# Kernel tuning notes

Hardware: AMD Instinct MI355X
Metric: run time of the kernel (lower is better)

The kernel has to match this reference:

```python
import jax, jax.numpy as jnp
import numpy as np

B, H_HIST, S_DIM, HID, G, K, A = 1024, 16384, 32, 64, 10, 4, 8


def setup_inputs() -> dict:
    key = jax.random.key(0)
    ks = jax.random.split(key, 12)
    inp = {
        'state_batch': jax.random.normal(ks[0], (B, S_DIM), jnp.float32),
        'state_history_batch': jax.random.normal(ks[1], (H_HIST, S_DIM), jnp.float32),
        'joint_action_history_batch': jax.random.normal(ks[2], (H_HIST, G, A), jnp.float32),
        # per-abstract-agent encoder MLP: Linear(S->H) + ReLU, Linear(H->H) + ReLU, Linear(H->H) + ReLU
        'W0': jax.random.normal(ks[3], (K, S_DIM, HID), jnp.float32) / np.sqrt(S_DIM),
        'b0': jax.random.normal(ks[4], (K, HID), jnp.float32) * 0.01,
        'W1': jax.random.normal(ks[5], (K, HID, HID), jnp.float32) / np.sqrt(HID),
        'b1': jax.random.normal(ks[6], (K, HID), jnp.float32) * 0.01,
        'W2': jax.random.normal(ks[7], (K, HID, HID), jnp.float32) / np.sqrt(HID),
        'b2': jax.random.normal(ks[8], (K, HID), jnp.float32) * 0.01,
        'assignment_matrix': jnp.ones((G, K), jnp.float32),
    }
    return inp


def _encode(x, W0, b0, W1, b1, W2, b2):
    # x: [N, S_DIM] shared across K encoders -> [K, N, HID]
    h = jax.nn.relu(jnp.einsum('ni,kio->kno', x, W0) + b0[:, None, :])
    h = jax.nn.relu(jnp.einsum('kni,kio->kno', h, W1) + b1[:, None, :])
    h = jax.nn.relu(jnp.einsum('kni,kio->kno', h, W2) + b2[:, None, :])
    return h


def reference(state_batch, state_history_batch, joint_action_history_batch,
              W0, b0, W1, b1, W2, b2, assignment_matrix):
    enc_s = _encode(state_batch, W0, b0, W1, b1, W2, b2)            # [K, B, HID]
    enc_h = _encode(state_history_batch, W0, b0, W1, b1, W2, b2)    # [K, H, HID]
    # per (abstract agent k, batch item b): softmax over history of <enc_h, enc_s>
    attn = jax.nn.softmax(jnp.einsum('khd,kbd->kbh', enc_h, enc_s), axis=-1)  # [K, B, H]
    # weighted action aggregation: [H,G,A] contracted over H
    abs_pred = jnp.einsum('kbh,hga->kbga', attn, joint_action_history_batch)  # [K, B, G, A]
    soft_assign = jax.nn.softmax(assignment_matrix, axis=-1)                  # [G, K]
    out = jnp.einsum('gk,kbga->bga', soft_assign, abs_pred)                   # [B, G, A]
    return out
```

## Files before the change

### kernel.cpp

```cpp
#include <hip/hip_runtime.h>
#include <stdint.h>

#define B_SZ 1024
#define H_SZ 16384
#define SD   32
#define HID  64
#define G_SZ 10
#define K_SZ 4
#define A_SZ 8
#define VA   80

typedef float f32x4  __attribute__((ext_vector_type(4)));
typedef short bf16x8 __attribute__((ext_vector_type(8)));

__device__ inline short f2bf(float a) {
    unsigned u = __float_as_uint(a);
    return (short)((u + 0x7FFFu + ((u >> 16) & 1u)) >> 16);
}
__device__ inline float bf2f(short s) {
    return __uint_as_float(((unsigned)(unsigned short)s) << 16);
}
__device__ inline void split_bf(float v, short& hi, short& lo) {
    hi = f2bf(v);
    lo = f2bf(v - bf2f(hi));
}
__device__ inline int pk_bf16(float a, float b) {
    unsigned ua = __float_as_uint(a), ub = __float_as_uint(b);
    ua = (ua + 0x7FFFu + ((ua >> 16) & 1u)) >> 16;
    ub = (ub + 0x7FFFu + ((ub >> 16) & 1u)) >> 16;
    return (int)(ua | (ub << 16));
}
__device__ inline void dma16(const short* g, const short* l) {
    __builtin_amdgcn_global_load_lds(
        (const __attribute__((address_space(1))) unsigned int*)g,
        (__attribute__((address_space(3))) unsigned int*)l, 16, 0, 0);
}

__global__ __launch_bounds__(256, 2) void k_encode(
    const float* __restrict__ state, const float* __restrict__ hist,
    const float* __restrict__ act,
    const float* __restrict__ W0, const float* __restrict__ b0,
    const float* __restrict__ W1, const float* __restrict__ b1,
    const float* __restrict__ W2, const float* __restrict__ b2,
    short* __restrict__ enc_s_h, short* __restrict__ enc_s_l,
    short* __restrict__ enc_h_h, short* __restrict__ enc_h_l,
    short* __restrict__ vt_h, short* __restrict__ vt_l)
{
    __shared__ __align__(16) short smem[28672];
    const int bid = blockIdx.x;
    const int t = threadIdx.x;

    if (bid >= 1088) {
        short* tile_h = smem;
        short* tile_l = smem + 10752;
        const int h0 = (bid - 1088) * 128;
        for (int i = 0; i < 40; ++i) {
            int idx = t + i * 256;
            float v = act[(size_t)h0 * VA + idx];
            int h = idx / VA, c = idx - h * VA;
            short hh, ll; split_bf(v, hh, ll);
            tile_h[h * 84 + c] = hh;
            tile_l[h * 84 + c] = ll;
        }
        __syncthreads();
        for (int i = 0; i < 5; ++i) {
            int j = t + i * 256;
            int va = j >> 4, hc = j & 15;
            union { short s[8]; uint4 v; } uh, ul;
            #pragma unroll
            for (int uu = 0; uu < 8; ++uu) {
                uh.s[uu] = tile_h[(hc * 8 + uu) * 84 + va];
                ul.s[uu] = tile_l[(hc * 8 + uu) * 84 + va];
            }
            int t32 = hc >> 2, g = hc & 3;
            int gp = g ^ ((va >> 1) & 3);
            *(uint4*)(vt_h + (size_t)va * H_SZ + h0 + t32 * 32 + gp * 8) = uh.v;
            *(uint4*)(vt_l + (size_t)va * H_SZ + h0 + t32 * 32 + gp * 8) = ul.v;
        }
        return;
    }

    const int k = bid / 272;
    const int tl = bid % 272;
    const bool swz = (tl >= 16);
    const float* X;
    short *dst_h, *dst_l;
    if (tl < 16) {
        X = state + (size_t)tl * 64 * SD;
        dst_h = enc_s_h + ((size_t)k * B_SZ + tl * 64) * HID;
        dst_l = enc_s_l + ((size_t)k * B_SZ + tl * 64) * HID;
    } else {
        X = hist + (size_t)(tl - 16) * 64 * SD;
        dst_h = enc_h_h + ((size_t)k * H_SZ + (tl - 16) * 64) * HID;
        dst_l = enc_h_l + ((size_t)k * H_SZ + (tl - 16) * 64) * HID;
    }

    short* xt_h  = smem;
    short* xt_l  = smem + 2560;
    short* wt0_h = smem + 5120;
    short* wt0_l = smem + 7680;
    short* hb2_h = smem;
    short* hb2_l = smem + 4608;
    short* wt1_h = smem + 10240;
    short* wt1_l = smem + 14848;
    short* hb1_h = smem + 19456;
    short* hb1_l = smem + 24064;
    short* wt2_h = smem + 19456;
    short* wt2_l = smem + 24064;

    const float* W0k = W0 + k * (SD * HID);
    const float* W1k = W1 + k * (HID * HID);
    const float* W2k = W2 + k * (HID * HID);

    {
        int r = t >> 2, c0 = (t & 3) * 8;
        const float* src = X + r * SD + c0;
        #pragma unroll
        for (int u = 0; u < 8; ++u) {
            short hh, ll; split_bf(src[u], hh, ll);
            xt_h[r * 40 + c0 + u] = hh;
            xt_l[r * 40 + c0 + u] = ll;
        }
    }
    {
        int i = t >> 3, j0 = (t & 7) * 8;
        #pragma unroll
        for (int u = 0; u < 8; ++u) {
            short hh, ll; split_bf(W0k[i * HID + j0 + u], hh, ll);
            wt0_h[(j0 + u) * 40 + i] = hh;
            wt0_l[(j0 + u) * 40 + i] = ll;
        }
    }
    {
        int i = t >> 2, j0 = (t & 3) * 16;
        #pragma unroll
        for (int u = 0; u < 16; ++u) {
            short hh, ll; split_bf(W1k[i * HID + j0 + u], hh, ll);
            wt1_h[(j0 + u) * 72 + i] = hh;
            wt1_l[(j0 + u) * 72 + i] = ll;
        }
    }
    __syncthreads();

    const int w = t >> 6, l15 = t & 15, quad = (t >> 4) & 3;
    const f32x4 fz = {0.f, 0.f, 0.f, 0.f};

    {
        bf16x8 xa_h = *(const bf16x8*)(xt_h + (w * 16 + l15) * 40 + quad * 8);
        bf16x8 xa_l = *(const bf16x8*)(xt_l + (w * 16 + l15) * 40 + quad * 8);
        const float* b0k = b0 + k * HID;
        #pragma unroll
        for (int tt = 0; tt < 4; ++tt) {
            bf16x8 wf_h = *(const bf16x8*)(wt0_h + (l15 + 16 * tt) * 40 + quad * 8);
            bf16x8 wf_l = *(const bf16x8*)(wt0_l + (l15 + 16 * tt) * 40 + quad * 8);
            f32x4 c = __builtin_amdgcn_mfma_f32_16x16x32_bf16(xa_h, wf_h, fz, 0, 0, 0);
            c = __builtin_amdgcn_mfma_f32_16x16x32_bf16(xa_l, wf_h, c, 0, 0, 0);
            c = __builtin_amdgcn_mfma_f32_16x16x32_bf16(xa_h, wf_l, c, 0, 0, 0);
            float bias = b0k[l15 + 16 * tt];
            #pragma unroll
            for (int r = 0; r < 4; ++r) {
                float f = fmaxf(c[r] + bias, 0.f);
                short hh, ll; split_bf(f, hh, ll);
                hb1_h[(w * 16 + quad * 4 + r) * 72 + l15 + 16 * tt] = hh;
                hb1_l[(w * 16 + quad * 4 + r) * 72 + l15 + 16 * tt] = ll;
            }
        }
    }
    __syncthreads();
    {
        bf16x8 ha0_h = *(const bf16x8*)(hb1_h + (w * 16 + l15) * 72 + quad * 8);
        bf16x8 ha0_l = *(const bf16x8*)(hb1_l + (w * 16 + l15) * 72 + quad * 8);
        bf16x8 ha1_h = *(const bf16x8*)(hb1_h + (w * 16 + l15) * 72 + 32 + quad * 8);
        bf16x8 ha1_l = *(const bf16x8*)(hb1_l + (w * 16 + l15) * 72 + 32 + quad * 8);
        const float* b1k = b1 + k * HID;
        #pragma unroll
        for (int tt = 0; tt < 4; ++tt) {
            bf16x8 wfa_h = *(const bf16x8*)(wt1_h + (l15 + 16 * tt) * 72 + quad * 8);
            bf16x8 wfa_l = *(const bf16x8*)(wt1_l + (l15 + 16 * tt) * 72 + quad * 8);
            bf16x8 wfb_h = *(const bf16x8*)(wt1_h + (l15 + 16 * tt) * 72 + 32 + quad * 8);
            bf16x8 wfb_l = *(const bf16x8*)(wt1_l + (l15 + 16 * tt) * 72 + 32 + quad * 8);
            f32x4 c = __builtin_amdgcn_mfma_f32_16x16x32_bf16(ha0_h, wfa_h, fz, 0, 0, 0);
            c = __builtin_amdgcn_mfma_f32_16x16x32_bf16(ha1_h, wfb_h, c, 0, 0, 0);
            c = __builtin_amdgcn_mfma_f32_16x16x32_bf16(ha0_l, wfa_h, c, 0, 0, 0);
            c = __builtin_amdgcn_mfma_f32_16x16x32_bf16(ha1_l, wfb_h, c, 0, 0, 0);
            c = __builtin_amdgcn_mfma_f32_16x16x32_bf16(ha0_h, wfa_l, c, 0, 0, 0);
            c = __builtin_amdgcn_mfma_f32_16x16x32_bf16(ha1_h, wfb_l, c, 0, 0, 0);
            float bias = b1k[l15 + 16 * tt];
            #pragma unroll
            for (int r = 0; r < 4; ++r) {
                float f = fmaxf(c[r] + bias, 0.f);
                short hh, ll; split_bf(f, hh, ll);
                hb2_h[(w * 16 + quad * 4 + r) * 72 + l15 + 16 * tt] = hh;
                hb2_l[(w * 16 + quad * 4 + r) * 72 + l15 + 16 * tt] = ll;
            }
        }
    }
    __syncthreads();
    {
        int i = t >> 2, j0 = (t & 3) * 16;
        #pragma unroll
        for (int u = 0; u < 16; ++u) {
            short hh, ll; split_bf(W2k[i * HID + j0 + u], hh, ll);
            wt2_h[(j0 + u) * 72 + i] = hh;
            wt2_l[(j0 + u) * 72 + i] = ll;
        }
    }
    __syncthreads();
    {
        bf16x8 ha0_h = *(const bf16x8*)(hb2_h + (w * 16 + l15) * 72 + quad * 8);
        bf16x8 ha0_l = *(const bf16x8*)(hb2_l + (w * 16 + l15) * 72 + quad * 8);
        bf16x8 ha1_h = *(const bf16x8*)(hb2_h + (w * 16 + l15) * 72 + 32 + quad * 8);
        bf16x8 ha1_l = *(const bf16x8*)(hb2_l + (w * 16 + l15) * 72 + 32 + quad * 8);
        const float* b2k = b2 + k * HID;
        #pragma unroll
        for (int tt = 0; tt < 4; ++tt) {
            bf16x8 wfa_h = *(const bf16x8*)(wt2_h + (l15 + 16 * tt) * 72 + quad * 8);
            bf16x8 wfa_l = *(const bf16x8*)(wt2_l + (l15 + 16 * tt) * 72 + quad * 8);
            bf16x8 wfb_h = *(const bf16x8*)(wt2_h + (l15 + 16 * tt) * 72 + 32 + quad * 8);
            bf16x8 wfb_l = *(const bf16x8*)(wt2_l + (l15 + 16 * tt) * 72 + 32 + quad * 8);
            f32x4 c = __builtin_amdgcn_mfma_f32_16x16x32_bf16(ha0_h, wfa_h, fz, 0, 0, 0);
            c = __builtin_amdgcn_mfma_f32_16x16x32_bf16(ha1_h, wfb_h, c, 0, 0, 0);
            c = __builtin_amdgcn_mfma_f32_16x16x32_bf16(ha0_l, wfa_h, c, 0, 0, 0);
            c = __builtin_amdgcn_mfma_f32_16x16x32_bf16(ha1_l, wfb_h, c, 0, 0, 0);
            c = __builtin_amdgcn_mfma_f32_16x16x32_bf16(ha0_h, wfa_l, c, 0, 0, 0);
            c = __builtin_amdgcn_mfma_f32_16x16x32_bf16(ha1_h, wfb_l, c, 0, 0, 0);
            float bias = b2k[l15 + 16 * tt];
            #pragma unroll
            for (int r = 0; r < 4; ++r) {
                float f = fmaxf(c[r] + bias, 0.f);
                short hh, ll; split_bf(f, hh, ll);
                int row = w * 16 + quad * 4 + r;
                int c0 = l15 + 16 * tt;
                int col = swz ? ((((c0 >> 3) ^ (row & 7)) << 3) | (c0 & 7)) : c0;
                dst_h[row * HID + col] = hh;
                dst_l[row * HID + col] = ll;
            }
        }
    }
}

template<int NCt>
__global__ __launch_bounds__(256, 4) void k_flash(
    const short* __restrict__ enc_s_h, const short* __restrict__ enc_s_l,
    const short* __restrict__ enc_h_h, const short* __restrict__ enc_h_l,
    const short* __restrict__ vth, const short* __restrict__ vtl,
    float* __restrict__ Pm, float* __restrict__ Pl, float* __restrict__ Pacc)
{
    constexpr int CHt = H_SZ / NCt;
    constexpr int NT = CHt / 32;
    __shared__ __align__(16) short kbh[2][32 * 64];
    __shared__ __align__(16) short kbl[2][32 * 64];
    __shared__ __align__(16) short vbh[2][80 * 32];
    __shared__ __align__(16) short vbl[2][80 * 32];

    const int bid = blockIdx.x;
    const int r8 = bid & 7, j = bid >> 3;
    const int mtile = j & 7, grp = j >> 3;
    const int idx = grp * 8 + r8;
    const int k = idx / NCt, chunk = idx % NCt;
    const int t = threadIdx.x, w = t >> 6, lane = t & 63;
    const int l15 = t & 15, quad = (t >> 4) & 3;
    const short* ehk_h = enc_h_h + (size_t)k * H_SZ * HID;
    const short* ehk_l = enc_h_l + (size_t)k * H_SZ * HID;
    const int h_base = chunk * CHt;
    const int q0 = mtile * 128 + w * 32;
    const float L2E = 1.44269504f;
    const f32x4 fz = {0.f, 0.f, 0.f, 0.f};

    bf16x8 qh[2][2], ql[2][2];
    #pragma unroll
    for (int sub = 0; sub < 2; ++sub)
        #pragma unroll
        for (int kb = 0; kb < 2; ++kb) {
            size_t off = ((size_t)k * B_SZ + q0 + sub * 16 + l15) * HID + kb * 32 + quad * 8;
            qh[sub][kb] = *(const bf16x8*)(enc_s_h + off);
            ql[sub][kb] = *(const bf16x8*)(enc_s_l + off);
        }

    f32x4 acc[2][5];
    #pragma unroll
    for (int s = 0; s < 2; ++s)
        #pragma unroll
        for (int tt = 0; tt < 5; ++tt) acc[s][tt] = fz;
    float mrun[2] = {-__builtin_inff(), -__builtin_inff()};
    float lrun[2] = {0.f, 0.f};

    const int koff0 = l15 * 64 + (((quad)     ^ (l15 & 7)) << 3);
    const int koff1 = l15 * 64 + (((4 + quad) ^ (l15 & 7)) << 3);
    const int vof   = l15 * 32 + ((quad ^ ((l15 >> 1) & 3)) << 3);

    auto vseg = [&](int seg, int h0, int nb) {
        bool hi = seg < 5;
        int sb = hi ? seg : seg - 5;
        int va = sb * 16 + (lane >> 2);
        const short* src = (hi ? vth : vtl) + (size_t)va * H_SZ + h0 + (lane & 3) * 8;
        const short* dst = (hi ? &vbh[nb][0] : &vbl[nb][0]) + sb * 512;
        dma16(src, dst);
    };
    auto stage = [&](int h0, int nb) {
        dma16(ehk_h + (size_t)h0 * 64 + w * 512 + lane * 8, &kbh[nb][w * 512]);
        dma16(ehk_l + (size_t)h0 * 64 + w * 512 + lane * 8, &kbl[nb][w * 512]);
        vseg(w, h0, nb);
        vseg(w + 4, h0, nb);
        if (w < 2) vseg(w + 8, h0, nb);
    };

    stage(h_base, 0);
    asm volatile("s_waitcnt vmcnt(0)" ::: "memory");
    __syncthreads();

    for (int it = 0; it < NT; ++it) {
        const int cur = it & 1;
        if (it + 1 < NT) stage(h_base + (it + 1) * 32, cur ^ 1);

        const short* kch = kbh[cur];
        const short* kcl = kbl[cur];
        const short* vch = vbh[cur];
        const short* vcl = vbl[cur];

        f32x4 S[2][2];
        __builtin_amdgcn_s_setprio(1);
        #pragma unroll
        for (int hs = 0; hs < 2; ++hs) {
            bf16x8 kah0 = *(const bf16x8*)(kch + hs * 1024 + koff0);
            bf16x8 kah1 = *(const bf16x8*)(kch + hs * 1024 + koff1);
            bf16x8 kal0 = *(const bf16x8*)(kcl + hs * 1024 + koff0);
            bf16x8 kal1 = *(const bf16x8*)(kcl + hs * 1024 + koff1);
            #pragma unroll
            for (int sub = 0; sub < 2; ++sub) {
                f32x4 c = __builtin_amdgcn_mfma_f32_16x16x32_bf16(kah0, qh[sub][0], fz, 0, 0, 0);
                c = __builtin_amdgcn_mfma_f32_16x16x32_bf16(kah1, qh[sub][1], c, 0, 0, 0);
                c = __builtin_amdgcn_mfma_f32_16x16x32_bf16(kal0, qh[sub][0], c, 0, 0, 0);
                c = __builtin_amdgcn_mfma_f32_16x16x32_bf16(kal1, qh[sub][1], c, 0, 0, 0);
                c = __builtin_amdgcn_mfma_f32_16x16x32_bf16(kah0, ql[sub][0], c, 0, 0, 0);
                c = __builtin_amdgcn_mfma_f32_16x16x32_bf16(kah1, ql[sub][1], c, 0, 0, 0);
                S[sub][hs] = c;
            }
        }
        __builtin_amdgcn_s_setprio(0);

        bf16x8 pfv[2];
        #pragma unroll
        for (int sub = 0; sub < 2; ++sub) {
            f32x4 slo = S[sub][0], shi = S[sub][1];
            float tm = fmaxf(fmaxf(fmaxf(slo[0], slo[1]), fmaxf(slo[2], slo[3])),
                             fmaxf(fmaxf(shi[0], shi[1]), fmaxf(shi[2], shi[3])));
            tm = fmaxf(tm, __shfl_xor(tm, 16));
            tm = fmaxf(tm, __shfl_xor(tm, 32));
            if (__any(tm > mrun[sub])) {
                float mnew = fmaxf(mrun[sub], tm);
                float alpha = exp2f((mrun[sub] - mnew) * L2E);
                lrun[sub] *= alpha;
                #pragma unroll
                for (int tt = 0; tt < 5; ++tt) acc[sub][tt] = acc[sub][tt] * alpha;
                mrun[sub] = mnew;
            }
            float m = mrun[sub];
            float p0 = exp2f((slo[0] - m) * L2E), p1 = exp2f((slo[1] - m) * L2E);
            float p2 = exp2f((slo[2] - m) * L2E), p3 = exp2f((slo[3] - m) * L2E);
            float p4 = exp2f((shi[0] - m) * L2E), p5 = exp2f((shi[1] - m) * L2E);
            float p6 = exp2f((shi[2] - m) * L2E), p7 = exp2f((shi[3] - m) * L2E);
            float ps = (p0 + p1) + (p2 + p3) + (p4 + p5) + (p6 + p7);
            ps += __shfl_xor(ps, 16);
            ps += __shfl_xor(ps, 32);
            lrun[sub] += ps;

            int plo01 = pk_bf16(p0, p1), plo23 = pk_bf16(p2, p3);
            int phi01 = pk_bf16(p4, p5), phi23 = pk_bf16(p6, p7);
            union { int i[4]; bf16x8 v; } pf;
            #pragma unroll
            for (int jj = 0; jj < 4; ++jj) {
                int src = (((2 * quad + (jj >> 1)) & 3) << 4) + l15;
                int glo = __shfl((jj & 1) ? plo23 : plo01, src);
                int ghi = __shfl((jj & 1) ? phi23 : phi01, src);
                pf.i[jj] = (quad >= 2) ? ghi : glo;
            }
            pfv[sub] = pf.v;
        }

        __builtin_amdgcn_s_setprio(1);
        #pragma unroll
        for (int tt = 0; tt < 5; ++tt) {
            bf16x8 vh = *(const bf16x8*)(vch + vof + tt * 512);
            bf16x8 vl = *(const bf16x8*)(vcl + vof + tt * 512);
            acc[0][tt] = __builtin_amdgcn_mfma_f32_16x16x32_bf16(vh, pfv[0], acc[0][tt], 0, 0, 0);
            acc[0][tt] = __builtin_amdgcn_mfma_f32_16x16x32_bf16(vl, pfv[0], acc[0][tt], 0, 0, 0);
            acc[1][tt] = __builtin_amdgcn_mfma_f32_16x16x32_bf16(vh, pfv[1], acc[1][tt], 0, 0, 0);
            acc[1][tt] = __builtin_amdgcn_mfma_f32_16x16x32_bf16(vl, pfv[1], acc[1][tt], 0, 0, 0);
        }
        __builtin_amdgcn_s_setprio(0);

        asm volatile("s_waitcnt vmcnt(0)" ::: "memory");
        __syncthreads();
    }

    const int qg = k * B_SZ + q0;
    #pragma unroll
    for (int sub = 0; sub < 2; ++sub) {
        int q = qg + sub * 16 + l15;
        if (quad == 0) {
            Pm[chunk * 4096 + q] = mrun[sub];
            Pl[chunk * 4096 + q] = lrun[sub];
        }
        #pragma unroll
        for (int tt = 0; tt < 5; ++tt)
            #pragma unroll
            for (int r = 0; r < 4; ++r) {
                int va = tt * 16 + quad * 4 + r;
                Pacc[((size_t)chunk * VA + va) * 4096 + q] = acc[sub][tt][r];
            }
    }
}

template<int NCt>
__global__ __launch_bounds__(256) void k_reduce1(
    const float* __restrict__ Pm, const float* __restrict__ Pl,
    const float* __restrict__ Pacc, float* __restrict__ O)
{
    const int bid = blockIdx.x;
    const int qb = bid / 10, vc = bid - qb * 10;
    const int t = threadIdx.x;
    const int q = qb * 64 + (t & 63);
    const int va0 = vc * 8 + (t >> 6) * 2;
    const float L2E = 1.44269504f;

    float mc[NCt];
    float M = -__builtin_inff();
    #pragma unroll
    for (int c = 0; c < NCt; ++c) { mc[c] = Pm[c * 4096 + q]; M = fmaxf(M, mc[c]); }
    float L = 0.f;
    float o0 = 0.f, o1 = 0.f;
    #pragma unroll
    for (int c = 0; c < NCt; ++c) {
        float wv = exp2f((mc[c] - M) * L2E);
        L += wv * Pl[c * 4096 + q];
        o0 += wv * Pacc[((size_t)c * VA + va0) * 4096 + q];
        o1 += wv * Pacc[((size_t)c * VA + va0 + 1) * 4096 + q];
    }
    float inv = 1.f / L;
    O[(size_t)q * VA + va0]     = o0 * inv;
    O[(size_t)q * VA + va0 + 1] = o1 * inv;
}

__global__ __launch_bounds__(256) void k_reduce2(
    const float* __restrict__ O, const float* __restrict__ assign,
    float* __restrict__ out)
{
    const int idx = blockIdx.x * 256 + threadIdx.x;
    const int b = idx / VA, va = idx - b * VA, g = va >> 3;
    const float L2E = 1.44269504f;
    float a0 = assign[g * K_SZ + 0], a1 = assign[g * K_SZ + 1];
    float a2 = assign[g * K_SZ + 2], a3 = assign[g * K_SZ + 3];
    float mx = fmaxf(fmaxf(a0, a1), fmaxf(a2, a3));
    float e0 = exp2f((a0 - mx) * L2E), e1 = exp2f((a1 - mx) * L2E);
    float e2 = exp2f((a2 - mx) * L2E), e3 = exp2f((a3 - mx) * L2E);
    float inv = 1.f / (e0 + e1 + e2 + e3);
    float o = e0 * O[((size_t)(0 * B_SZ + b)) * VA + va]
            + e1 * O[((size_t)(1 * B_SZ + b)) * VA + va]
            + e2 * O[((size_t)(2 * B_SZ + b)) * VA + va]
            + e3 * O[((size_t)(3 * B_SZ + b)) * VA + va];
    out[idx] = o * inv;
}

extern "C" void kernel_launch(void* const* d_in, const int* in_sizes, int n_in,
                              void* d_out, int out_size, void* d_ws, size_t ws_size,
                              hipStream_t stream)
{
    const float* state  = (const float*)d_in[0];
    const float* hist   = (const float*)d_in[1];
    const float* act    = (const float*)d_in[2];
    const float* W0     = (const float*)d_in[3];
    const float* b0     = (const float*)d_in[4];
    const float* W1     = (const float*)d_in[5];
    const float* b1     = (const float*)d_in[6];
    const float* W2     = (const float*)d_in[7];
    const float* b2     = (const float*)d_in[8];
    const float* assign = (const float*)d_in[9];
    float* out = (float*)d_out;

    char* ws = (char*)d_ws;
    short* enc_s_h = (short*)(ws);
    short* enc_s_l = (short*)(ws + 524288);
    short* enc_h_h = (short*)(ws + 1048576);
    short* enc_h_l = (short*)(ws + 9437184);
    short* vt_h    = (short*)(ws + 17825792);
    short* vt_l    = (short*)(ws + 20447232);
    const size_t base = 23068672;

    const size_t need32 = base + 32ull * (32768 + 1310720) + 1310720;
    const int nc = (ws_size >= need32) ? 32 : 16;

    float* Pm   = (float*)(ws + base);
    float* Pl   = (float*)(ws + base + (size_t)nc * 16384);
    float* Pacc = (float*)(ws + base + (size_t)nc * 32768);
    float* O    = (float*)(ws + base + (size_t)nc * 32768 + (size_t)nc * 1310720);

    k_encode<<<1216, 256, 0, stream>>>(state, hist, act, W0, b0, W1, b1, W2, b2,
                                       enc_s_h, enc_s_l, enc_h_h, enc_h_l, vt_h, vt_l);
    if (nc == 32) {
        k_flash<32><<<1024, 256, 0, stream>>>(enc_s_h, enc_s_l, enc_h_h, enc_h_l,
                                              vt_h, vt_l, Pm, Pl, Pacc);
        k_reduce1<32><<<640, 256, 0, stream>>>(Pm, Pl, Pacc, O);
    } else {
        k_flash<16><<<512, 256, 0, stream>>>(enc_s_h, enc_s_l, enc_h_h, enc_h_l,
                                             vt_h, vt_l, Pm, Pl, Pacc);
        k_reduce1<16><<<640, 256, 0, stream>>>(Pm, Pl, Pacc, O);
    }
    k_reduce2<<<320, 256, 0, stream>>>(O, assign, out);
}
```

Before: 183.4 us.

## Store K/V in MFMA fragment order and load directly to registers

The encoder now writes history encodings and transposed actions straight into a per-lane MFMA fragment layout. The flash kernel drops its LDS double-buffered DMA staging and barriers and loads operands from global memory into registers with one contiguous 16-byte load per lane. A new small prep kernel pre-splits and transposes the weights into bf16 hi/lo once, so encoder blocks copy them instead of converting. The trade-off is that the flash kernel loses explicit prefetch overlap and relies on cache and wave-level latency hiding, with occupancy lowered to 3 blocks, plus one extra kernel launch.

```diff
diff --git a/kernel.cpp b/kernel.cpp
--- a/kernel.cpp
+++ b/kernel.cpp
@@ -30,21 +30,44 @@
     ub = (ub + 0x7FFFu + ((ub >> 16) & 1u)) >> 16;
     return (int)(ua | (ub << 16));
 }
-__device__ inline void dma16(const short* g, const short* l) {
-    __builtin_amdgcn_global_load_lds(
-        (const __attribute__((address_space(1))) unsigned int*)g,
-        (__attribute__((address_space(3))) unsigned int*)l, 16, 0, 0);
+
+__global__ __launch_bounds__(256) void k_prep(
+    const float* __restrict__ W0, const float* __restrict__ W1,
+    const float* __restrict__ W2,
+    short* __restrict__ w0h, short* __restrict__ w0l,
+    short* __restrict__ w1h, short* __restrict__ w1l,
+    short* __restrict__ w2h, short* __restrict__ w2l)
+{
+    int idx = blockIdx.x * 256 + threadIdx.x;
+    short hh, ll;
+    if (idx < 8192) {
+        int k = idx >> 11, j = (idx >> 5) & 63, i = idx & 31;
+        split_bf(W0[k * 2048 + i * 64 + j], hh, ll);
+        w0h[idx] = hh; w0l[idx] = ll;
+    } else if (idx < 24576) {
+        int d = idx - 8192;
+        int k = d >> 12, j = (d >> 6) & 63, i = d & 63;
+        split_bf(W1[k * 4096 + i * 64 + j], hh, ll);
+        w1h[d] = hh; w1l[d] = ll;
+    } else if (idx < 40960) {
+        int d = idx - 24576;
+        int k = d >> 12, j = (d >> 6) & 63, i = d & 63;
+        split_bf(W2[k * 4096 + i * 64 + j], hh, ll);
+        w2h[d] = hh; w2l[d] = ll;
+    }
 }
 
 __global__ __launch_bounds__(256, 2) void k_encode(
     const float* __restrict__ state, const float* __restrict__ hist,
     const float* __restrict__ act,
-    const float* __restrict__ W0, const float* __restrict__ b0,
-    const float* __restrict__ W1, const float* __restrict__ b1,
-    const float* __restrict__ W2, const float* __restrict__ b2,
+    const short* __restrict__ w0th, const short* __restrict__ w0tl,
+    const short* __restrict__ w1th, const short* __restrict__ w1tl,
+    const short* __restrict__ w2th, const short* __restrict__ w2tl,
+    const float* __restrict__ b0, const float* __restrict__ b1,
+    const float* __restrict__ b2,
     short* __restrict__ enc_s_h, short* __restrict__ enc_s_l,
-    short* __restrict__ enc_h_h, short* __restrict__ enc_h_l,
-    short* __restrict__ vt_h, short* __restrict__ vt_l)
+    short* __restrict__ kf_h, short* __restrict__ kf_l,
+    short* __restrict__ vf_h, short* __restrict__ vf_l)
 {
     __shared__ __align__(16) short smem[28672];
     const int bid = blockIdx.x;
@@ -72,28 +95,28 @@
                 uh.s[uu] = tile_h[(hc * 8 + uu) * 84 + va];
                 ul.s[uu] = tile_l[(hc * 8 + uu) * 84 + va];
             }
-            int t32 = hc >> 2, g = hc & 3;
-            int gp = g ^ ((va >> 1) & 3);
-            *(uint4*)(vt_h + (size_t)va * H_SZ + h0 + t32 * 32 + gp * 8) = uh.v;
-            *(uint4*)(vt_l + (size_t)va * H_SZ + h0 + t32 * 32 + gp * 8) = ul.v;
+            int vtile = (h0 >> 5) + (hc >> 2);
+            int lanep = ((hc & 3) << 4) | (va & 15);
+            size_t a = (size_t)vtile * 2560 + (va >> 4) * 512 + lanep * 8;
+            *(uint4*)(vf_h + a) = uh.v;
+            *(uint4*)(vf_l + a) = ul.v;
         }
         return;
     }
 
     const int k = bid / 272;
     const int tl = bid % 272;
-    const bool swz = (tl >= 16);
+    const bool is_state = (tl < 16);
     const float* X;
-    short *dst_h, *dst_l;
-    if (tl < 16) {
+    short *dst_h = nullptr, *dst_l = nullptr;
+    if (is_state) {
         X = state + (size_t)tl * 64 * SD;
         dst_h = enc_s_h + ((size_t)k * B_SZ + tl * 64) * HID;
         dst_l = enc_s_l + ((size_t)k * B_SZ + tl * 64) * HID;
     } else {
         X = hist + (size_t)(tl - 16) * 64 * SD;
-        dst_h = enc_h_h + ((size_t)k * H_SZ + (tl - 16) * 64) * HID;
-        dst_l = enc_h_l + ((size_t)k * H_SZ + (tl - 16) * 64) * HID;
-    }
+    }
+    const int hbase64 = (tl - 16) * 64;
 
     short* xt_h  = smem;
     short* xt_l  = smem + 2560;
@@ -108,10 +131,6 @@
     short* wt2_h = smem + 19456;
     short* wt2_l = smem + 24064;
 
-    const float* W0k = W0 + k * (SD * HID);
-    const float* W1k = W1 + k * (HID * HID);
-    const float* W2k = W2 + k * (HID * HID);
-
     {
         int r = t >> 2, c0 = (t & 3) * 8;
         const float* src = X + r * SD + c0;
@@ -123,22 +142,16 @@
         }
     }
     {
-        int i = t >> 3, j0 = (t & 7) * 8;
-        #pragma unroll
-        for (int u = 0; u < 8; ++u) {
-            short hh, ll; split_bf(W0k[i * HID + j0 + u], hh, ll);
-            wt0_h[(j0 + u) * 40 + i] = hh;
-            wt0_l[(j0 + u) * 40 + i] = ll;
-        }
-    }
-    {
-        int i = t >> 2, j0 = (t & 3) * 16;
-        #pragma unroll
-        for (int u = 0; u < 16; ++u) {
-            short hh, ll; split_bf(W1k[i * HID + j0 + u], hh, ll);
-            wt1_h[(j0 + u) * 72 + i] = hh;
-            wt1_l[(j0 + u) * 72 + i] = ll;
-        }
+        int jj = t >> 2, i0 = (t & 3) * 8;
+        *(uint4*)(wt0_h + jj * 40 + i0) = *(const uint4*)(w0th + k * 2048 + jj * 32 + i0);
+        *(uint4*)(wt0_l + jj * 40 + i0) = *(const uint4*)(w0tl + k * 2048 + jj * 32 + i0);
+    }
+    {
+        int jj = t >> 2, i0 = (t & 3) * 16;
+        *(uint4*)(wt1_h + jj * 72 + i0)     = *(const uint4*)(w1th + k * 4096 + jj * 64 + i0);
+        *(uint4*)(wt1_h + jj * 72 + i0 + 8) = *(const uint4*)(w1th + k * 4096 + jj * 64 + i0 + 8);
+        *(uint4*)(wt1_l + jj * 72 + i0)     = *(const uint4*)(w1tl + k * 4096 + jj * 64 + i0);
+        *(uint4*)(wt1_l + jj * 72 + i0 + 8) = *(const uint4*)(w1tl + k * 4096 + jj * 64 + i0 + 8);
     }
     __syncthreads();
 
@@ -197,13 +210,11 @@
     }
     __syncthreads();
     {
-        int i = t >> 2, j0 = (t & 3) * 16;
-        #pragma unroll
-        for (int u = 0; u < 16; ++u) {
-            short hh, ll; split_bf(W2k[i * HID + j0 + u], hh, ll);
-            wt2_h[(j0 + u) * 72 + i] = hh;
-            wt2_l[(j0 + u) * 72 + i] = ll;
-        }
+        int jj = t >> 2, i0 = (t & 3) * 16;
+        *(uint4*)(wt2_h + jj * 72 + i0)     = *(const uint4*)(w2th + k * 4096 + jj * 64 + i0);
+        *(uint4*)(wt2_h + jj * 72 + i0 + 8) = *(const uint4*)(w2th + k * 4096 + jj * 64 + i0 + 8);
+        *(uint4*)(wt2_l + jj * 72 + i0)     = *(const uint4*)(w2tl + k * 4096 + jj * 64 + i0);
+        *(uint4*)(wt2_l + jj * 72 + i0 + 8) = *(const uint4*)(w2tl + k * 4096 + jj * 64 + i0 + 8);
     }
     __syncthreads();
     {
@@ -230,28 +241,33 @@
                 float f = fmaxf(c[r] + bias, 0.f);
                 short hh, ll; split_bf(f, hh, ll);
                 int row = w * 16 + quad * 4 + r;
-                int c0 = l15 + 16 * tt;
-                int col = swz ? ((((c0 >> 3) ^ (row & 7)) << 3) | (c0 & 7)) : c0;
-                dst_h[row * HID + col] = hh;
-                dst_l[row * HID + col] = ll;
+                int col = l15 + 16 * tt;
+                if (is_state) {
+                    dst_h[row * HID + col] = hh;
+                    dst_l[row * HID + col] = ll;
+                } else {
+                    int hg = hbase64 + row;
+                    int ktile = k * 512 + (hg >> 5);
+                    int f2 = ((hg >> 4) & 1) * 2 + (col >> 5);
+                    int lanep = (((col >> 3) & 3) << 4) | (hg & 15);
+                    size_t a = (size_t)ktile * 2048 + f2 * 512 + lanep * 8 + (col & 7);
+                    kf_h[a] = hh;
+                    kf_l[a] = ll;
+                }
             }
         }
     }
 }
 
 template<int NCt>
-__global__ __launch_bounds__(256, 4) void k_flash(
+__global__ __launch_bounds__(256, 3) void k_flash(
     const short* __restrict__ enc_s_h, const short* __restrict__ enc_s_l,
-    const short* __restrict__ enc_h_h, const short* __restrict__ enc_h_l,
-    const short* __restrict__ vth, const short* __restrict__ vtl,
+    const short* __restrict__ kf_h, const short* __restrict__ kf_l,
+    const short* __restrict__ vf_h, const short* __restrict__ vf_l,
     float* __restrict__ Pm, float* __restrict__ Pl, float* __restrict__ Pacc)
 {
     constexpr int CHt = H_SZ / NCt;
     constexpr int NT = CHt / 32;
-    __shared__ __align__(16) short kbh[2][32 * 64];
-    __shared__ __align__(16) short kbl[2][32 * 64];
-    __shared__ __align__(16) short vbh[2][80 * 32];
-    __shared__ __align__(16) short vbl[2][80 * 32];
 
     const int bid = blockIdx.x;
     const int r8 = bid & 7, j = bid >> 3;
@@ -260,9 +276,6 @@
     const int k = idx / NCt, chunk = idx % NCt;
     const int t = threadIdx.x, w = t >> 6, lane = t & 63;
     const int l15 = t & 15, quad = (t >> 4) & 3;
-    const short* ehk_h = enc_h_h + (size_t)k * H_SZ * HID;
-    const short* ehk_l = enc_h_l + (size_t)k * H_SZ * HID;
-    const int h_base = chunk * CHt;
     const int q0 = mtile * 128 + w * 32;
     const float L2E = 1.44269504f;
     const f32x4 fz = {0.f, 0.f, 0.f, 0.f};
@@ -285,57 +298,40 @@
     float mrun[2] = {-__builtin_inff(), -__builtin_inff()};
     float lrun[2] = {0.f, 0.f};
 
-    const int koff0 = l15 * 64 + (((quad)     ^ (l15 & 7)) << 3);
-    const int koff1 = l15 * 64 + (((4 + quad) ^ (l15 & 7)) << 3);
-    const int vof   = l15 * 32 + ((quad ^ ((l15 >> 1) & 3)) << 3);
-
-    auto vseg = [&](int seg, int h0, int nb) {
-        bool hi = seg < 5;
-        int sb = hi ? seg : seg - 5;
-        int va = sb * 16 + (lane >> 2);
-        const short* src = (hi ? vth : vtl) + (size_t)va * H_SZ + h0 + (lane & 3) * 8;
-        const short* dst = (hi ? &vbh[nb][0] : &vbl[nb][0]) + sb * 512;
-        dma16(src, dst);
-    };
-    auto stage = [&](int h0, int nb) {
-        dma16(ehk_h + (size_t)h0 * 64 + w * 512 + lane * 8, &kbh[nb][w * 512]);
-        dma16(ehk_l + (size_t)h0 * 64 + w * 512 + lane * 8, &kbl[nb][w * 512]);
-        vseg(w, h0, nb);
-        vseg(w + 4, h0, nb);
-        if (w < 2) vseg(w + 8, h0, nb);
-    };
-
-    stage(h_base, 0);
-    asm volatile("s_waitcnt vmcnt(0)" ::: "memory");
-    __syncthreads();
+    const int tile0 = chunk * NT;
+    const short* kth = kf_h + ((size_t)(k * 512 + tile0)) * 2048 + lane * 8;
+    const short* ktl = kf_l + ((size_t)(k * 512 + tile0)) * 2048 + lane * 8;
+    const short* vth = vf_h + (size_t)tile0 * 2560 + lane * 8;
+    const short* vtl = vf_l + (size_t)tile0 * 2560 + lane * 8;
 
     for (int it = 0; it < NT; ++it) {
-        const int cur = it & 1;
-        if (it + 1 < NT) stage(h_base + (it + 1) * 32, cur ^ 1);
-
-        const short* kch = kbh[cur];
-        const short* kcl = kbl[cur];
-        const short* vch = vbh[cur];
-        const short* vcl = vbl[cur];
+        bf16x8 kah0 = *(const bf16x8*)(kth + 0 * 512);
+        bf16x8 kah1 = *(const bf16x8*)(kth + 1 * 512);
+        bf16x8 kah2 = *(const bf16x8*)(kth + 2 * 512);
+        bf16x8 kah3 = *(const bf16x8*)(kth + 3 * 512);
+        bf16x8 kal0 = *(const bf16x8*)(ktl + 0 * 512);
+        bf16x8 kal1 = *(const bf16x8*)(ktl + 1 * 512);
+        bf16x8 kal2 = *(const bf16x8*)(ktl + 2 * 512);
+        bf16x8 kal3 = *(const bf16x8*)(ktl + 3 * 512);
 
         f32x4 S[2][2];
         __builtin_amdgcn_s_setprio(1);
         #pragma unroll
-        for (int hs = 0; hs < 2; ++hs) {
-            bf16x8 kah0 = *(const bf16x8*)(kch + hs * 1024 + koff0);
-            bf16x8 kah1 = *(const bf16x8*)(kch + hs * 1024 + koff1);
-            bf16x8 kal0 = *(const bf16x8*)(kcl + hs * 1024 + koff0);
-            bf16x8 kal1 = *(const bf16x8*)(kcl + hs * 1024 + koff1);
-            #pragma unroll
-            for (int sub = 0; sub < 2; ++sub) {
-                f32x4 c = __builtin_amdgcn_mfma_f32_16x16x32_bf16(kah0, qh[sub][0], fz, 0, 0, 0);
-                c = __builtin_amdgcn_mfma_f32_16x16x32_bf16(kah1, qh[sub][1], c, 0, 0, 0);
-                c = __builtin_amdgcn_mfma_f32_16x16x32_bf16(kal0, qh[sub][0], c, 0, 0, 0);
-                c = __builtin_amdgcn_mfma_f32_16x16x32_bf16(kal1, qh[sub][1], c, 0, 0, 0);
-                c = __builtin_amdgcn_mfma_f32_16x16x32_bf16(kah0, ql[sub][0], c, 0, 0, 0);
-                c = __builtin_amdgcn_mfma_f32_16x16x32_bf16(kah1, ql[sub][1], c, 0, 0, 0);
-                S[sub][hs] = c;
-            }
+        for (int sub = 0; sub < 2; ++sub) {
+            f32x4 c = __builtin_amdgcn_mfma_f32_16x16x32_bf16(kah0, qh[sub][0], fz, 0, 0, 0);
+            c = __builtin_amdgcn_mfma_f32_16x16x32_bf16(kah1, qh[sub][1], c, 0, 0, 0);
+            c = __builtin_amdgcn_mfma_f32_16x16x32_bf16(kal0, qh[sub][0], c, 0, 0, 0);
+            c = __builtin_amdgcn_mfma_f32_16x16x32_bf16(kal1, qh[sub][1], c, 0, 0, 0);
+            c = __builtin_amdgcn_mfma_f32_16x16x32_bf16(kah0, ql[sub][0], c, 0, 0, 0);
+            c = __builtin_amdgcn_mfma_f32_16x16x32_bf16(kah1, ql[sub][1], c, 0, 0, 0);
+            S[sub][0] = c;
+            f32x4 d = __builtin_amdgcn_mfma_f32_16x16x32_bf16(kah2, qh[sub][0], fz, 0, 0, 0);
+            d = __builtin_amdgcn_mfma_f32_16x16x32_bf16(kah3, qh[sub][1], d, 0, 0, 0);
+            d = __builtin_amdgcn_mfma_f32_16x16x32_bf16(kal2, qh[sub][0], d, 0, 0, 0);
+            d = __builtin_amdgcn_mfma_f32_16x16x32_bf16(kal3, qh[sub][1], d, 0, 0, 0);
+            d = __builtin_amdgcn_mfma_f32_16x16x32_bf16(kah2, ql[sub][0], d, 0, 0, 0);
+            d = __builtin_amdgcn_mfma_f32_16x16x32_bf16(kah3, ql[sub][1], d, 0, 0, 0);
+            S[sub][1] = d;
         }
         __builtin_amdgcn_s_setprio(0);
 
@@ -381,8 +377,8 @@
         __builtin_amdgcn_s_setprio(1);
         #pragma unroll
         for (int tt = 0; tt < 5; ++tt) {
-            bf16x8 vh = *(const bf16x8*)(vch + vof + tt * 512);
-            bf16x8 vl = *(const bf16x8*)(vcl + vof + tt * 512);
+            bf16x8 vh = *(const bf16x8*)(vth + tt * 512);
+            bf16x8 vl = *(const bf16x8*)(vtl + tt * 512);
             acc[0][tt] = __builtin_amdgcn_mfma_f32_16x16x32_bf16(vh, pfv[0], acc[0][tt], 0, 0, 0);
             acc[0][tt] = __builtin_amdgcn_mfma_f32_16x16x32_bf16(vl, pfv[0], acc[0][tt], 0, 0, 0);
             acc[1][tt] = __builtin_amdgcn_mfma_f32_16x16x32_bf16(vh, pfv[1], acc[1][tt], 0, 0, 0);
@@ -390,8 +386,8 @@
         }
         __builtin_amdgcn_s_setprio(0);
 
-        asm volatile("s_waitcnt vmcnt(0)" ::: "memory");
-        __syncthreads();
+        kth += 2048; ktl += 2048;
+        vth += 2560; vtl += 2560;
     }
 
     const int qg = k * B_SZ + q0;
@@ -481,29 +477,39 @@
     char* ws = (char*)d_ws;
     short* enc_s_h = (short*)(ws);
     short* enc_s_l = (short*)(ws + 524288);
-    short* enc_h_h = (short*)(ws + 1048576);
-    short* enc_h_l = (short*)(ws + 9437184);
-    short* vt_h    = (short*)(ws + 17825792);
-    short* vt_l    = (short*)(ws + 20447232);
+    short* kf_h    = (short*)(ws + 1048576);
+    short* kf_l    = (short*)(ws + 9437184);
+    short* vf_h    = (short*)(ws + 17825792);
+    short* vf_l    = (short*)(ws + 20447232);
     const size_t base = 23068672;
 
-    const size_t need32 = base + 32ull * (32768 + 1310720) + 1310720;
+    const size_t need32 = base + 32ull * (32768 + 1310720) + 1310720 + 163840;
     const int nc = (ws_size >= need32) ? 32 : 16;
 
     float* Pm   = (float*)(ws + base);
     float* Pl   = (float*)(ws + base + (size_t)nc * 16384);
     float* Pacc = (float*)(ws + base + (size_t)nc * 32768);
     float* O    = (float*)(ws + base + (size_t)nc * 32768 + (size_t)nc * 1310720);
-
-    k_encode<<<1216, 256, 0, stream>>>(state, hist, act, W0, b0, W1, b1, W2, b2,
-                                       enc_s_h, enc_s_l, enc_h_h, enc_h_l, vt_h, vt_l);
+    char*  wt   = (char*)O + 1310720;
+    short* w0th = (short*)(wt);
+    short* w0tl = (short*)(wt + 16384);
+    short* w1th = (short*)(wt + 32768);
+    short* w1tl = (short*)(wt + 65536);
+    short* w2th = (short*)(wt + 98304);
+    short* w2tl = (short*)(wt + 131072);
+
+    k_prep<<<160, 256, 0, stream>>>(W0, W1, W2, w0th, w0tl, w1th, w1tl, w2th, w2tl);
+    k_encode<<<1216, 256, 0, stream>>>(state, hist, act,
+                                       w0th, w0tl, w1th, w1tl, w2th, w2tl,
+                                       b0, b1, b2,
+                                       enc_s_h, enc_s_l, kf_h, kf_l, vf_h, vf_l);
     if (nc == 32) {
-        k_flash<32><<<1024, 256, 0, stream>>>(enc_s_h, enc_s_l, enc_h_h, enc_h_l,
-                                              vt_h, vt_l, Pm, Pl, Pacc);
+        k_flash<32><<<1024, 256, 0, stream>>>(enc_s_h, enc_s_l, kf_h, kf_l,
+                                              vf_h, vf_l, Pm, Pl, Pacc);
         k_reduce1<32><<<640, 256, 0, stream>>>(Pm, Pl, Pacc, O);
     } else {
-        k_flash<16><<<512, 256, 0, stream>>>(enc_s_h, enc_s_l, enc_h_h, enc_h_l,
-                                             vt_h, vt_l, Pm, Pl, Pacc);
+        k_flash<16><<<512, 256, 0, stream>>>(enc_s_h, enc_s_l, kf_h, kf_l,
+                                             vf_h, vf_l, Pm, Pl, Pacc);
         k_reduce1<16><<<640, 256, 0, stream>>>(Pm, Pl, Pacc, O);
     }
     k_reduce2<<<320, 256, 0, stream>>>(O, assign, out);
```

Measured after the change: 205.4 us. 12.0% more time.
